# Kernel tuning notes

Hardware: AMD Instinct MI355X
Metric: run time of the kernel (lower is better)

Reference implementation:

```python
import jax, jax.numpy as jnp
import numpy as np

N = 50000        # nodes
E = 800000       # edges
H = 128          # in = hidden = out width
L = 4            # num_layers
BN_EPS = 1e-5


def _bn(x, g, b):
    # training-mode batch norm over the node dimension (biased variance, as torch)
    mu = jnp.mean(x, axis=0)
    var = jnp.mean((x - mu) ** 2, axis=0)
    return (x - mu) * jax.lax.rsqrt(var + BN_EPS) * g + b


def setup_inputs() -> dict:
    key = jax.random.key(0)
    ks = jax.random.split(key, 16)
    s = 0.05
    return {
        "x": jax.random.normal(ks[0], (N, H), dtype=jnp.float32),
        "edge_index": jax.random.randint(ks[1], (2, E), 0, N, dtype=jnp.int32),
        # stacked per-layer MLP params (all layers share dims H->H->H)
        "fc1_w": jax.random.normal(ks[2], (L, H, H), dtype=jnp.float32) * s,
        "fc1_b": jnp.zeros((L, H), dtype=jnp.float32),
        "bn1_g": jnp.ones((L, H), dtype=jnp.float32),
        "bn1_b": jnp.zeros((L, H), dtype=jnp.float32),
        "fc2_w": jax.random.normal(ks[3], (L, H, H), dtype=jnp.float32) * s,
        "fc2_b": jnp.zeros((L, H), dtype=jnp.float32),
        "bn2_g": jnp.ones((L, H), dtype=jnp.float32),
        "bn2_b": jnp.zeros((L, H), dtype=jnp.float32),
        # outer per-layer BatchNorm (intended one-per-GIN-layer)
        "bn3_g": jnp.ones((L, H), dtype=jnp.float32),
        "bn3_b": jnp.zeros((L, H), dtype=jnp.float32),
        # final classifier
        "fc_w": jax.random.normal(ks[4], (H, H), dtype=jnp.float32) * s,
        "fc_b": jnp.zeros((H,), dtype=jnp.float32),
    }


def reference(x, edge_index, fc1_w, fc1_b, bn1_g, bn1_b, fc2_w, fc2_b,
              bn2_g, bn2_b, bn3_g, bn3_b, fc_w, fc_b):
    src = edge_index[0]
    dst = edge_index[1]
    for i in range(L):
        # GINConv, eps=0: h = MLP((1+eps)*x + sum_{j in N(v)} x_j)
        agg = jax.ops.segment_sum(x[src], dst, num_segments=N)  # [N, H]
        h = x + agg
        # MLP: relu(bn1(fc1(h))) -> bn2(fc2(.))
        h = jax.nn.relu(_bn(h @ fc1_w[i].T + fc1_b[i], bn1_g[i], bn1_b[i]))
        h = _bn(h @ fc2_w[i].T + fc2_b[i], bn2_g[i], bn2_b[i])
        # outer BN + ReLU per layer
        x = jax.nn.relu(_bn(h, bn3_g[i], bn3_b[i]))
    return x @ fc_w.T + fc_b  # [N, H]
```

## Files before the change

### kernel.cpp

```cpp
#include <hip/hip_runtime.h>

#define NN 50000
#define HD 128
#define NL 4
#define BN_EPS 1e-5f
#define NTILES 3125
#define MAXDEG 64

typedef __attribute__((ext_vector_type(8))) short short8;
typedef __attribute__((ext_vector_type(4))) float f32x4;
typedef __attribute__((ext_vector_type(4))) uint uint4v;

__device__ inline ushort f2bf(float f){
  uint u = __float_as_uint(f);
  uint r = (u + 0x7fffu + ((u >> 16) & 1u)) >> 16;
  return (ushort)r;
}
__device__ inline float bflo(uint u){ return __uint_as_float(u << 16); }
__device__ inline float bfhi(uint u){ return __uint_as_float(u & 0xffff0000u); }
__device__ inline uint pk2(float lo, float hi){
  return (uint)f2bf(lo) | ((uint)f2bf(hi) << 16);
}

__global__ __launch_bounds__(256) void cast_all(const float* __restrict__ x,
                                                const float* __restrict__ w1,
                                                const float* __restrict__ w2,
                                                const float* __restrict__ wf,
                                                ushort* __restrict__ xb,
                                                ushort* __restrict__ wb){
  const int NX = NN * HD / 4;
  const int NT = NX + 36864;
  int i = blockIdx.x * 256 + threadIdx.x;
  int stride = gridDim.x * 256;
  for (; i < NT; i += stride){
    const float* src; ushort* dst;
    if (i < NX){ src = x + i * 4; dst = xb + i * 4; }
    else {
      int k = i - NX;
      dst = wb + k * 4;
      if (k < 16384)      src = w1 + k * 4;
      else if (k < 32768) src = w2 + (k - 16384) * 4;
      else                src = wf + (k - 32768) * 4;
    }
    float4 v = *(const float4*)src;
    ushort4 r;
    r.x = f2bf(v.x); r.y = f2bf(v.y); r.z = f2bf(v.z); r.w = f2bf(v.w);
    *(ushort4*)dst = r;
  }
}

__global__ void fill1_kernel(const int* __restrict__ dst, int* __restrict__ cnt,
                             int* __restrict__ pos, int E){
  int e = (blockIdx.x * 256 + threadIdx.x) * 4;
  if (e + 4 <= E){
    int4 d = *(const int4*)(dst + e);
    int4 p;
    p.x = atomicAdd(&cnt[d.x], 1);
    p.y = atomicAdd(&cnt[d.y], 1);
    p.z = atomicAdd(&cnt[d.z], 1);
    p.w = atomicAdd(&cnt[d.w], 1);
    *(int4*)(pos + e) = p;
  } else {
    for (; e < E; ++e) pos[e] = atomicAdd(&cnt[dst[e]], 1);
  }
}

__global__ void fill2_kernel(const int* __restrict__ src, const int* __restrict__ dst,
                             const int* __restrict__ pos, int* __restrict__ slots, int E){
  int e = (blockIdx.x * 256 + threadIdx.x) * 4;
  if (e + 4 <= E){
    int4 d = *(const int4*)(dst + e);
    int4 p = *(const int4*)(pos + e);
    int4 s = *(const int4*)(src + e);
    slots[d.x * MAXDEG + p.x] = s.x;
    slots[d.y * MAXDEG + p.y] = s.y;
    slots[d.z * MAXDEG + p.z] = s.z;
    slots[d.w * MAXDEG + p.w] = s.w;
  } else {
    for (; e < E; ++e) slots[dst[e] * MAXDEG + pos[e]] = src[e];
  }
}

__device__ inline void bn_params8(const float* __restrict__ st, const float* __restrict__ gA,
                                  const float* __restrict__ gB, const float* __restrict__ bB,
                                  int mode, float* sS, float* sT){
  int c = threadIdx.x;
  if (c < 128){
    float s0 = 0.f, s1 = 0.f;
#pragma unroll
    for (int k = 0; k < 8; ++k){
      s0 += st[k * 256 + c];
      s1 += st[k * 256 + 128 + c];
    }
    const float invN = 1.f / (float)NN;
    float mu = s0 * invN;
    float var = fmaxf(s1 * invN - mu * mu, 0.f);
    float S, T;
    if (mode == 0){
      S = gA[c] * rsqrtf(var + BN_EPS);
      T = gB[c] - mu * S;
    } else {
      float inv2 = rsqrtf(var + BN_EPS);
      float tt = gA[c] * inv2;
      float inv3 = rsqrtf(tt * tt * var + BN_EPS);
      S = tt * inv3 * gB[c];
      T = bB[c] - mu * S;
    }
    sS[c] = S; sT[c] = T;
  }
}

template<bool AFF>
__global__ __launch_bounds__(512, 6) void aggemm_t(const ushort* __restrict__ xin,
                                                   const int* __restrict__ deg,
                                                   const int* __restrict__ slots,
                                                   const ushort* __restrict__ W,
                                                   const float* __restrict__ bias,
                                                   ushort* __restrict__ Yb,
                                                   float* __restrict__ statsOut,
                                                   const float* __restrict__ statsIn,
                                                   const float* __restrict__ g2,
                                                   const float* __restrict__ g3,
                                                   const float* __restrict__ b3){
  __shared__ uint4v w4[128 * 17];
  __shared__ uint4v a4[2][16 * 17];
  __shared__ float ssum[128];
  __shared__ float ssq[128];
  __shared__ float sS[128];
  __shared__ float sT[128];

  const uint4v* Wg = (const uint4v*)W;
  for (int c = threadIdx.x; c < 2048; c += 512){
    w4[(c >> 4) * 17 + (c & 15)] = Wg[c];
  }
  if (AFF) bn_params8(statsIn, g2, g3, b3, 1, sS, sT);
  if (threadIdx.x < 128){ ssum[threadIdx.x] = 0.f; ssq[threadIdx.x] = 0.f; }
  __syncthreads();

  int wave = threadIdx.x >> 6;
  int lane = threadIdx.x & 63;
  int tl   = wave >> 2;
  int qd   = wave & 3;
  int grp  = lane >> 4;
  int col  = lane & 15;
  int tile = blockIdx.x * 2 + tl;
  bool tv = tile < NTILES;

  float S[8], T[8];
  if (AFF){
#pragma unroll
    for (int k = 0; k < 8; ++k){ S[k] = sS[col * 8 + k]; T[k] = sT[col * 8 + k]; }
  }

  const uint4v* x4 = (const uint4v*)xin;

#define ACC8(v)                                                                 \
  if (AFF){                                                                     \
    a[0]+=fmaxf(bflo((v).x)*S[0]+T[0],0.f); a[1]+=fmaxf(bfhi((v).x)*S[1]+T[1],0.f); \
    a[2]+=fmaxf(bflo((v).y)*S[2]+T[2],0.f); a[3]+=fmaxf(bfhi((v).y)*S[3]+T[3],0.f); \
    a[4]+=fmaxf(bflo((v).z)*S[4]+T[4],0.f); a[5]+=fmaxf(bfhi((v).z)*S[5]+T[5],0.f); \
    a[6]+=fmaxf(bflo((v).w)*S[6]+T[6],0.f); a[7]+=fmaxf(bfhi((v).w)*S[7]+T[7],0.f); \
  } else {                                                                      \
    a[0]+=bflo((v).x); a[1]+=bfhi((v).x); a[2]+=bflo((v).y); a[3]+=bfhi((v).y); \
    a[4]+=bflo((v).z); a[5]+=bfhi((v).z); a[6]+=bflo((v).w); a[7]+=bfhi((v).w); \
  }

  if (tv){
    int node = tile * 16 + qd * 4 + grp;
    int e = deg[node];
    const int* sl = slots + node * MAXDEG;
    float a[8];
    {
      uint4v v = x4[node * 16 + col];
      if (AFF){
        a[0]=fmaxf(bflo(v.x)*S[0]+T[0],0.f); a[1]=fmaxf(bfhi(v.x)*S[1]+T[1],0.f);
        a[2]=fmaxf(bflo(v.y)*S[2]+T[2],0.f); a[3]=fmaxf(bfhi(v.y)*S[3]+T[3],0.f);
        a[4]=fmaxf(bflo(v.z)*S[4]+T[4],0.f); a[5]=fmaxf(bfhi(v.z)*S[5]+T[5],0.f);
        a[6]=fmaxf(bflo(v.w)*S[6]+T[6],0.f); a[7]=fmaxf(bfhi(v.w)*S[7]+T[7],0.f);
      } else {
        a[0]=bflo(v.x); a[1]=bfhi(v.x); a[2]=bflo(v.y); a[3]=bfhi(v.y);
        a[4]=bflo(v.z); a[5]=bfhi(v.z); a[6]=bflo(v.w); a[7]=bfhi(v.w);
      }
    }
    int j = 0;
    for (; j + 8 <= e; j += 8){
      int i0 = sl[j+0], i1 = sl[j+1], i2 = sl[j+2], i3 = sl[j+3];
      int i4 = sl[j+4], i5 = sl[j+5], i6 = sl[j+6], i7 = sl[j+7];
      uint4v v0 = x4[i0 * 16 + col];
      uint4v v1 = x4[i1 * 16 + col];
      uint4v v2 = x4[i2 * 16 + col];
      uint4v v3 = x4[i3 * 16 + col];
      uint4v v4 = x4[i4 * 16 + col];
      uint4v v5 = x4[i5 * 16 + col];
      uint4v v6 = x4[i6 * 16 + col];
      uint4v v7 = x4[i7 * 16 + col];
      ACC8(v0); ACC8(v1); ACC8(v2); ACC8(v3);
      ACC8(v4); ACC8(v5); ACC8(v6); ACC8(v7);
    }
    for (; j + 4 <= e; j += 4){
      int i0 = sl[j+0], i1 = sl[j+1], i2 = sl[j+2], i3 = sl[j+3];
      uint4v v0 = x4[i0 * 16 + col];
      uint4v v1 = x4[i1 * 16 + col];
      uint4v v2 = x4[i2 * 16 + col];
      uint4v v3 = x4[i3 * 16 + col];
      ACC8(v0); ACC8(v1); ACC8(v2); ACC8(v3);
    }
    for (; j < e; ++j){
      uint4v v = x4[sl[j] * 16 + col];
      ACC8(v);
    }
    uint4v o;
    o.x = pk2(a[0], a[1]); o.y = pk2(a[2], a[3]);
    o.z = pk2(a[4], a[5]); o.w = pk2(a[6], a[7]);
    a4[tl][(qd * 4 + grp) * 17 + col] = o;
  }
#undef ACC8
  __syncthreads();

  int m = lane & 15, q = lane >> 4;
  f32x4 acc[2];
  acc[0] = (f32x4)0.f; acc[1] = (f32x4)0.f;

#pragma unroll
  for (int kt = 0; kt < 4; ++kt){
    uint4v t = a4[tl][m * 17 + kt * 4 + q];
    short8 af = *(short8*)&t;
#pragma unroll
    for (int t2 = 0; t2 < 2; ++t2){
      int to = qd * 2 + t2;
      uint4v bw = w4[(to * 16 + m) * 17 + kt * 4 + q];
      acc[t2] = __builtin_amdgcn_mfma_f32_16x16x32_bf16(af, *(short8*)&bw, acc[t2], 0, 0, 0);
    }
  }

#pragma unroll
  for (int t2 = 0; t2 < 2; ++t2){
    int colo = (qd * 2 + t2) * 16 + m;
    float bc = bias[colo];
    float ls = 0.f, lq = 0.f;
    if (tv){
#pragma unroll
      for (int r = 0; r < 4; ++r){
        float v = acc[t2][r] + bc;
        int row = tile * 16 + q * 4 + r;
        __builtin_nontemporal_store(__builtin_bit_cast(ushort, f2bf(v)), Yb + row * 128 + colo);
        ls += v; lq += v * v;
      }
    }
    ls += __shfl_xor(ls, 16); lq += __shfl_xor(lq, 16);
    ls += __shfl_xor(ls, 32); lq += __shfl_xor(lq, 32);
    if (tv && q == 0){ atomicAdd(&ssum[colo], ls); atomicAdd(&ssq[colo], lq); }
  }
  __syncthreads();
  if (threadIdx.x < 128){
    int sb = (blockIdx.x & 7) * 256;
    atomicAdd(&statsOut[sb + threadIdx.x], ssum[threadIdx.x]);
    atomicAdd(&statsOut[sb + 128 + threadIdx.x], ssq[threadIdx.x]);
  }
}

__global__ __launch_bounds__(512, 8) void gemm_kernel(const ushort* __restrict__ A,
                                                   const ushort* __restrict__ W,
                                                   const float* __restrict__ bias,
                                                   ushort* __restrict__ Yb,
                                                   float* __restrict__ Yf,
                                                   float* __restrict__ statsOut,
                                                   const float* __restrict__ statsIn,
                                                   const float* __restrict__ gA,
                                                   const float* __restrict__ gB,
                                                   const float* __restrict__ bB,
                                                   int mode){
  __shared__ uint4v w4[128 * 17];
  __shared__ float ssum[128];
  __shared__ float ssq[128];
  __shared__ float sS[128];
  __shared__ float sT[128];
  const uint4v* Wg = (const uint4v*)W;
  for (int c = threadIdx.x; c < 2048; c += 512){
    w4[(c >> 4) * 17 + (c & 15)] = Wg[c];
  }
  if (statsIn) bn_params8(statsIn, gA, gB, bB, mode, sS, sT);
  if (threadIdx.x < 128){ ssum[threadIdx.x] = 0.f; ssq[threadIdx.x] = 0.f; }
  __syncthreads();

  int wave = threadIdx.x >> 6;
  int lane = threadIdx.x & 63;
  int m = lane & 15, q = lane >> 4;
  int tl   = wave >> 1;
  int half = wave & 1;
  int tile = blockIdx.x * 4 + tl;
  bool tv = tile < NTILES;
  const uint4v* A4 = (const uint4v*)A;

  f32x4 acc[4];
#pragma unroll
  for (int i = 0; i < 4; ++i) acc[i] = (f32x4)0.f;

#pragma unroll
  for (int kt = 0; kt < 4; ++kt){
    short8 af = (short8)0;
    if (tv){
      uint4v t = __builtin_nontemporal_load(A4 + (tile * 16 + m) * 16 + kt * 4 + q);
      if (statsIn){
        int kc = kt * 32 + q * 8;
        uint4v pk;
        pk.x = pk2(fmaxf(bflo(t.x)*sS[kc+0]+sT[kc+0],0.f),
                   fmaxf(bfhi(t.x)*sS[kc+1]+sT[kc+1],0.f));
        pk.y = pk2(fmaxf(bflo(t.y)*sS[kc+2]+sT[kc+2],0.f),
                   fmaxf(bfhi(t.y)*sS[kc+3]+sT[kc+3],0.f));
        pk.z = pk2(fmaxf(bflo(t.z)*sS[kc+4]+sT[kc+4],0.f),
                   fmaxf(bfhi(t.z)*sS[kc+5]+sT[kc+5],0.f));
        pk.w = pk2(fmaxf(bflo(t.w)*sS[kc+6]+sT[kc+6],0.f),
                   fmaxf(bfhi(t.w)*sS[kc+7]+sT[kc+7],0.f));
        t = pk;
      }
      af = *(short8*)&t;
    }
#pragma unroll
    for (int t4 = 0; t4 < 4; ++t4){
      int to = half * 4 + t4;
      uint4v bw = w4[(to * 16 + m) * 17 + kt * 4 + q];
      acc[t4] = __builtin_amdgcn_mfma_f32_16x16x32_bf16(af, *(short8*)&bw, acc[t4], 0, 0, 0);
    }
  }

  bool dost = (statsOut != nullptr);
#pragma unroll
  for (int t4 = 0; t4 < 4; ++t4){
    int col = (half * 4 + t4) * 16 + m;
    float bc = bias[col];
    float ls = 0.f, lq = 0.f;
    if (tv){
#pragma unroll
      for (int r = 0; r < 4; ++r){
        float v = acc[t4][r] + bc;
        int row = tile * 16 + q * 4 + r;
        if (Yb) __builtin_nontemporal_store(__builtin_bit_cast(ushort, f2bf(v)), Yb + row * 128 + col);
        else    __builtin_nontemporal_store(v, Yf + row * 128 + col);
        ls += v; lq += v * v;
      }
    }
    if (dost){
      ls += __shfl_xor(ls, 16); lq += __shfl_xor(lq, 16);
      ls += __shfl_xor(ls, 32); lq += __shfl_xor(lq, 32);
      if (tv && q == 0){ atomicAdd(&ssum[col], ls); atomicAdd(&ssq[col], lq); }
    }
  }
  if (dost){
    __syncthreads();
    if (threadIdx.x < 128){
      int sb = (blockIdx.x & 7) * 256;
      atomicAdd(&statsOut[sb + threadIdx.x], ssum[threadIdx.x]);
      atomicAdd(&statsOut[sb + 128 + threadIdx.x], ssq[threadIdx.x]);
    }
  }
}

extern "C" void kernel_launch(void* const* d_in, const int* in_sizes, int n_in,
                              void* d_out, int out_size, void* d_ws, size_t ws_size,
                              hipStream_t stream) {
  const float* x     = (const float*)d_in[0];
  const int*   ei    = (const int*)d_in[1];
  const float* fc1_w = (const float*)d_in[2];
  const float* fc1_b = (const float*)d_in[3];
  const float* bn1_g = (const float*)d_in[4];
  const float* bn1_b = (const float*)d_in[5];
  const float* fc2_w = (const float*)d_in[6];
  const float* fc2_b = (const float*)d_in[7];
  const float* bn2_g = (const float*)d_in[8];
  const float* bn3_g = (const float*)d_in[10];
  const float* bn3_b = (const float*)d_in[11];
  const float* fc_w  = (const float*)d_in[12];
  const float* fc_b  = (const float*)d_in[13];

  int E = in_sizes[1] / 2;
  const int* srcp = ei;
  const int* dstp = ei + E;

  char* ws = (char*)d_ws;
  int*    cnt    = (int*)(ws + 0);
  float*  stats  = (float*)(ws + 200064);
  int*    pos    = (int*)(ws + 265600);
  int*    slots  = (int*)(ws + 3465600);
  ushort* wb     = (ushort*)(ws + 16265600);
  ushort* xb     = (ushort*)(ws + 16560512);
  ushort* y1b    = (ushort*)(ws + 29360512);
  ushort* y2b    = (ushort*)(ws + 42160512);

  hipMemsetAsync(ws, 0, 265600, stream);

  cast_all<<<2048, 256, 0, stream>>>(x, fc1_w, fc2_w, fc_w, xb, wb);

  const int EB4 = (E / 4 + 255) / 256 + 1;
  fill1_kernel<<<EB4, 256, 0, stream>>>(dstp, cnt, pos, E);
  fill2_kernel<<<EB4, 256, 0, stream>>>(srcp, dstp, pos, slots, E);

  const int ga = (NTILES + 1) / 2;
  const int gb = (NTILES + 3) / 4;

  for (int i = 0; i < NL; ++i){
    if (i == 0){
      aggemm_t<false><<<ga, 512, 0, stream>>>(xb, cnt, slots, wb + i * 16384,
                                              fc1_b + i * 128, y1b,
                                              stats + (i * 2) * 2048,
                                              nullptr, nullptr, nullptr, nullptr);
    } else {
      aggemm_t<true><<<ga, 512, 0, stream>>>(y2b, cnt, slots, wb + i * 16384,
                                             fc1_b + i * 128, y1b,
                                             stats + (i * 2) * 2048,
                                             stats + ((i - 1) * 2 + 1) * 2048,
                                             bn2_g + (i - 1) * 128,
                                             bn3_g + (i - 1) * 128,
                                             bn3_b + (i - 1) * 128);
    }
    gemm_kernel<<<gb, 512, 0, stream>>>(y1b, wb + 65536 + i * 16384, fc2_b + i * 128,
                                        y2b, nullptr, stats + (i * 2 + 1) * 2048,
                                        stats + (i * 2) * 2048, bn1_g + i * 128,
                                        bn1_b + i * 128, nullptr, 0);
  }

  gemm_kernel<<<gb, 512, 0, stream>>>(y2b, wb + 131072, fc_b,
                                      nullptr, (float*)d_out, nullptr,
                                      stats + 7 * 2048, bn2_g + 384,
                                      bn3_g + 384, bn3_b + 384, 1);
}
```

Before: 467.7 us.

## Split aggregation from GEMM and store features in column-sliced layout

The fused aggregate+GEMM kernel becomes a standalone gather kernel. It works on four 32-column slices of a sliced feature layout, so each slice's gathered rows are compact and likely to stay cache-resident. The fc1 GEMM now runs as a separate gemm_kernel launch that reads the sliced layout. The fc2 GEMM writes its output sliced for the next layer's gather. Stats binning grows from 8 to 64 bins to reduce atomic contention. The cost is an extra kernel launch per layer and an extra round trip of the aggregated features through memory.

After: 512.2 us. 1.1x slower.

```diff
diff --git a/kernel.cpp b/kernel.cpp
--- a/kernel.cpp
+++ b/kernel.cpp
@@ -6,6 +6,7 @@
 #define BN_EPS 1e-5f
 #define NTILES 3125
 #define MAXDEG 64
+#define SBIN 64
 
 typedef __attribute__((ext_vector_type(8))) short short8;
 typedef __attribute__((ext_vector_type(4))) float f32x4;
@@ -26,7 +27,7 @@
                                                 const float* __restrict__ w1,
                                                 const float* __restrict__ w2,
                                                 const float* __restrict__ wf,
-                                                ushort* __restrict__ xb,
+                                                ushort* __restrict__ xs,
                                                 ushort* __restrict__ wb){
   const int NX = NN * HD / 4;
   const int NT = NX + 36864;
@@ -34,8 +35,12 @@
   int stride = gridDim.x * 256;
   for (; i < NT; i += stride){
     const float* src; ushort* dst;
-    if (i < NX){ src = x + i * 4; dst = xb + i * 4; }
-    else {
+    if (i < NX){
+      int node = i >> 5;
+      int c0 = (i & 31) * 4;
+      src = x + i * 4;
+      dst = xs + ((c0 >> 5) * NN + node) * 32 + (c0 & 31);
+    } else {
       int k = i - NX;
       dst = wb + k * 4;
       if (k < 16384)      src = w1 + k * 4;
@@ -81,14 +86,14 @@
   }
 }
 
-__device__ inline void bn_params8(const float* __restrict__ st, const float* __restrict__ gA,
-                                  const float* __restrict__ gB, const float* __restrict__ bB,
-                                  int mode, float* sS, float* sT){
+__device__ inline void bn_params(const float* __restrict__ st, const float* __restrict__ gA,
+                                 const float* __restrict__ gB, const float* __restrict__ bB,
+                                 int mode, float* sS, float* sT){
   int c = threadIdx.x;
   if (c < 128){
     float s0 = 0.f, s1 = 0.f;
-#pragma unroll
-    for (int k = 0; k < 8; ++k){
+#pragma unroll 8
+    for (int k = 0; k < SBIN; ++k){
       s0 += st[k * 256 + c];
       s1 += st[k * 256 + 128 + c];
     }
@@ -111,152 +116,90 @@
 }
 
 template<bool AFF>
-__global__ __launch_bounds__(512, 6) void aggemm_t(const ushort* __restrict__ xin,
-                                                   const int* __restrict__ deg,
-                                                   const int* __restrict__ slots,
-                                                   const ushort* __restrict__ W,
-                                                   const float* __restrict__ bias,
-                                                   ushort* __restrict__ Yb,
-                                                   float* __restrict__ statsOut,
-                                                   const float* __restrict__ statsIn,
-                                                   const float* __restrict__ g2,
-                                                   const float* __restrict__ g3,
-                                                   const float* __restrict__ b3){
-  __shared__ uint4v w4[128 * 17];
-  __shared__ uint4v a4[2][16 * 17];
-  __shared__ float ssum[128];
-  __shared__ float ssq[128];
+__global__ __launch_bounds__(256) void aggs_t(const ushort* __restrict__ xs,
+                                              const int* __restrict__ deg,
+                                              const int* __restrict__ slots,
+                                              const float* __restrict__ statsIn,
+                                              const float* __restrict__ g2,
+                                              const float* __restrict__ g3,
+                                              const float* __restrict__ b3,
+                                              ushort* __restrict__ hs){
   __shared__ float sS[128];
   __shared__ float sT[128];
-
-  const uint4v* Wg = (const uint4v*)W;
-  for (int c = threadIdx.x; c < 2048; c += 512){
-    w4[(c >> 4) * 17 + (c & 15)] = Wg[c];
-  }
-  if (AFF) bn_params8(statsIn, g2, g3, b3, 1, sS, sT);
-  if (threadIdx.x < 128){ ssum[threadIdx.x] = 0.f; ssq[threadIdx.x] = 0.f; }
-  __syncthreads();
-
-  int wave = threadIdx.x >> 6;
-  int lane = threadIdx.x & 63;
-  int tl   = wave >> 2;
-  int qd   = wave & 3;
-  int grp  = lane >> 4;
-  int col  = lane & 15;
-  int tile = blockIdx.x * 2 + tl;
-  bool tv = tile < NTILES;
+  if (AFF){
+    bn_params(statsIn, g2, g3, b3, 1, sS, sT);
+    __syncthreads();
+  }
+  int slice = blockIdx.x & 3;
+  int nb    = blockIdx.x >> 2;
+  int gid   = threadIdx.x >> 2;
+  int li    = threadIdx.x & 3;
+  int node  = nb * 64 + gid;
+  if (node >= NN) return;
 
   float S[8], T[8];
   if (AFF){
-#pragma unroll
-    for (int k = 0; k < 8; ++k){ S[k] = sS[col * 8 + k]; T[k] = sT[col * 8 + k]; }
-  }
-
-  const uint4v* x4 = (const uint4v*)xin;
-
-#define ACC8(v)                                                                 \
-  if (AFF){                                                                     \
+    int cb = slice * 32 + li * 8;
+#pragma unroll
+    for (int k = 0; k < 8; ++k){ S[k] = sS[cb + k]; T[k] = sT[cb + k]; }
+  }
+
+  const uint4v* x4 = (const uint4v*)xs;
+  const int base = slice * (NN * 4);
+  int e = deg[node];
+  const int* sl = slots + node * MAXDEG;
+
+  float a[8];
+#define UNPK(v)                                                                  \
+  if (AFF){                                                                      \
     a[0]+=fmaxf(bflo((v).x)*S[0]+T[0],0.f); a[1]+=fmaxf(bfhi((v).x)*S[1]+T[1],0.f); \
     a[2]+=fmaxf(bflo((v).y)*S[2]+T[2],0.f); a[3]+=fmaxf(bfhi((v).y)*S[3]+T[3],0.f); \
     a[4]+=fmaxf(bflo((v).z)*S[4]+T[4],0.f); a[5]+=fmaxf(bfhi((v).z)*S[5]+T[5],0.f); \
     a[6]+=fmaxf(bflo((v).w)*S[6]+T[6],0.f); a[7]+=fmaxf(bfhi((v).w)*S[7]+T[7],0.f); \
-  } else {                                                                      \
-    a[0]+=bflo((v).x); a[1]+=bfhi((v).x); a[2]+=bflo((v).y); a[3]+=bfhi((v).y); \
-    a[4]+=bflo((v).z); a[5]+=bfhi((v).z); a[6]+=bflo((v).w); a[7]+=bfhi((v).w); \
-  }
-
-  if (tv){
-    int node = tile * 16 + qd * 4 + grp;
-    int e = deg[node];
-    const int* sl = slots + node * MAXDEG;
-    float a[8];
-    {
-      uint4v v = x4[node * 16 + col];
-      if (AFF){
-        a[0]=fmaxf(bflo(v.x)*S[0]+T[0],0.f); a[1]=fmaxf(bfhi(v.x)*S[1]+T[1],0.f);
-        a[2]=fmaxf(bflo(v.y)*S[2]+T[2],0.f); a[3]=fmaxf(bfhi(v.y)*S[3]+T[3],0.f);
-        a[4]=fmaxf(bflo(v.z)*S[4]+T[4],0.f); a[5]=fmaxf(bfhi(v.z)*S[5]+T[5],0.f);
-        a[6]=fmaxf(bflo(v.w)*S[6]+T[6],0.f); a[7]=fmaxf(bfhi(v.w)*S[7]+T[7],0.f);
-      } else {
-        a[0]=bflo(v.x); a[1]=bfhi(v.x); a[2]=bflo(v.y); a[3]=bfhi(v.y);
-        a[4]=bflo(v.z); a[5]=bfhi(v.z); a[6]=bflo(v.w); a[7]=bfhi(v.w);
-      }
-    }
-    int j = 0;
-    for (; j + 8 <= e; j += 8){
-      int i0 = sl[j+0], i1 = sl[j+1], i2 = sl[j+2], i3 = sl[j+3];
-      int i4 = sl[j+4], i5 = sl[j+5], i6 = sl[j+6], i7 = sl[j+7];
-      uint4v v0 = x4[i0 * 16 + col];
-      uint4v v1 = x4[i1 * 16 + col];
-      uint4v v2 = x4[i2 * 16 + col];
-      uint4v v3 = x4[i3 * 16 + col];
-      uint4v v4 = x4[i4 * 16 + col];
-      uint4v v5 = x4[i5 * 16 + col];
-      uint4v v6 = x4[i6 * 16 + col];
-      uint4v v7 = x4[i7 * 16 + col];
-      ACC8(v0); ACC8(v1); ACC8(v2); ACC8(v3);
-      ACC8(v4); ACC8(v5); ACC8(v6); ACC8(v7);
-    }
-    for (; j + 4 <= e; j += 4){
-      int i0 = sl[j+0], i1 = sl[j+1], i2 = sl[j+2], i3 = sl[j+3];
-      uint4v v0 = x4[i0 * 16 + col];
-      uint4v v1 = x4[i1 * 16 + col];
-      uint4v v2 = x4[i2 * 16 + col];
-      uint4v v3 = x4[i3 * 16 + col];
-      ACC8(v0); ACC8(v1); ACC8(v2); ACC8(v3);
-    }
-    for (; j < e; ++j){
-      uint4v v = x4[sl[j] * 16 + col];
-      ACC8(v);
-    }
-    uint4v o;
-    o.x = pk2(a[0], a[1]); o.y = pk2(a[2], a[3]);
-    o.z = pk2(a[4], a[5]); o.w = pk2(a[6], a[7]);
-    a4[tl][(qd * 4 + grp) * 17 + col] = o;
-  }
-#undef ACC8
-  __syncthreads();
-
-  int m = lane & 15, q = lane >> 4;
-  f32x4 acc[2];
-  acc[0] = (f32x4)0.f; acc[1] = (f32x4)0.f;
-
-#pragma unroll
-  for (int kt = 0; kt < 4; ++kt){
-    uint4v t = a4[tl][m * 17 + kt * 4 + q];
-    short8 af = *(short8*)&t;
-#pragma unroll
-    for (int t2 = 0; t2 < 2; ++t2){
-      int to = qd * 2 + t2;
-      uint4v bw = w4[(to * 16 + m) * 17 + kt * 4 + q];
-      acc[t2] = __builtin_amdgcn_mfma_f32_16x16x32_bf16(af, *(short8*)&bw, acc[t2], 0, 0, 0);
-    }
-  }
-
-#pragma unroll
-  for (int t2 = 0; t2 < 2; ++t2){
-    int colo = (qd * 2 + t2) * 16 + m;
-    float bc = bias[colo];
-    float ls = 0.f, lq = 0.f;
-    if (tv){
-#pragma unroll
-      for (int r = 0; r < 4; ++r){
-        float v = acc[t2][r] + bc;
-        int row = tile * 16 + q * 4 + r;
-        __builtin_nontemporal_store(__builtin_bit_cast(ushort, f2bf(v)), Yb + row * 128 + colo);
-        ls += v; lq += v * v;
-      }
-    }
-    ls += __shfl_xor(ls, 16); lq += __shfl_xor(lq, 16);
-    ls += __shfl_xor(ls, 32); lq += __shfl_xor(lq, 32);
-    if (tv && q == 0){ atomicAdd(&ssum[colo], ls); atomicAdd(&ssq[colo], lq); }
-  }
-  __syncthreads();
-  if (threadIdx.x < 128){
-    int sb = (blockIdx.x & 7) * 256;
-    atomicAdd(&statsOut[sb + threadIdx.x], ssum[threadIdx.x]);
-    atomicAdd(&statsOut[sb + 128 + threadIdx.x], ssq[threadIdx.x]);
-  }
+  } else {                                                                       \
+    a[0]+=bflo((v).x); a[1]+=bfhi((v).x); a[2]+=bflo((v).y); a[3]+=bfhi((v).y);  \
+    a[4]+=bflo((v).z); a[5]+=bfhi((v).z); a[6]+=bflo((v).w); a[7]+=bfhi((v).w);  \
+  }
+
+#pragma unroll
+  for (int k = 0; k < 8; ++k) a[k] = 0.f;
+  {
+    uint4v v = x4[base + node * 4 + li];
+    UNPK(v);
+  }
+  int j = 0;
+  for (; j + 8 <= e; j += 8){
+    int i0 = sl[j+0], i1 = sl[j+1], i2 = sl[j+2], i3 = sl[j+3];
+    int i4 = sl[j+4], i5 = sl[j+5], i6 = sl[j+6], i7 = sl[j+7];
+    uint4v v0 = x4[base + i0 * 4 + li];
+    uint4v v1 = x4[base + i1 * 4 + li];
+    uint4v v2 = x4[base + i2 * 4 + li];
+    uint4v v3 = x4[base + i3 * 4 + li];
+    uint4v v4 = x4[base + i4 * 4 + li];
+    uint4v v5 = x4[base + i5 * 4 + li];
+    uint4v v6 = x4[base + i6 * 4 + li];
+    uint4v v7 = x4[base + i7 * 4 + li];
+    UNPK(v0); UNPK(v1); UNPK(v2); UNPK(v3);
+    UNPK(v4); UNPK(v5); UNPK(v6); UNPK(v7);
+  }
+  for (; j + 4 <= e; j += 4){
+    int i0 = sl[j+0], i1 = sl[j+1], i2 = sl[j+2], i3 = sl[j+3];
+    uint4v v0 = x4[base + i0 * 4 + li];
+    uint4v v1 = x4[base + i1 * 4 + li];
+    uint4v v2 = x4[base + i2 * 4 + li];
+    uint4v v3 = x4[base + i3 * 4 + li];
+    UNPK(v0); UNPK(v1); UNPK(v2); UNPK(v3);
+  }
+  for (; j < e; ++j){
+    uint4v v = x4[base + sl[j] * 4 + li];
+    UNPK(v);
+  }
+#undef UNPK
+
+  uint4v o;
+  o.x = pk2(a[0], a[1]); o.y = pk2(a[2], a[3]);
+  o.z = pk2(a[4], a[5]); o.w = pk2(a[6], a[7]);
+  __builtin_nontemporal_store(o, (uint4v*)hs + base + node * 4 + li);
 }
 
 __global__ __launch_bounds__(512, 8) void gemm_kernel(const ushort* __restrict__ A,
@@ -269,7 +212,7 @@
                                                    const float* __restrict__ gA,
                                                    const float* __restrict__ gB,
                                                    const float* __restrict__ bB,
-                                                   int mode){
+                                                   int mode, int isl, int osl){
   __shared__ uint4v w4[128 * 17];
   __shared__ float ssum[128];
   __shared__ float ssq[128];
@@ -279,7 +222,7 @@
   for (int c = threadIdx.x; c < 2048; c += 512){
     w4[(c >> 4) * 17 + (c & 15)] = Wg[c];
   }
-  if (statsIn) bn_params8(statsIn, gA, gB, bB, mode, sS, sT);
+  if (statsIn) bn_params(statsIn, gA, gB, bB, mode, sS, sT);
   if (threadIdx.x < 128){ ssum[threadIdx.x] = 0.f; ssq[threadIdx.x] = 0.f; }
   __syncthreads();
 
@@ -296,13 +239,17 @@
 #pragma unroll
   for (int i = 0; i < 4; ++i) acc[i] = (f32x4)0.f;
 
+  int row = tile * 16 + m;
 #pragma unroll
   for (int kt = 0; kt < 4; ++kt){
     short8 af = (short8)0;
     if (tv){
-      uint4v t = __builtin_nontemporal_load(A4 + (tile * 16 + m) * 16 + kt * 4 + q);
+      int c = kt * 4 + q;
+      const uint4v* ap = isl ? (A4 + ((c >> 2) * (NN * 4) + row * 4 + (c & 3)))
+                             : (A4 + row * 16 + c);
+      uint4v t = __builtin_nontemporal_load(ap);
       if (statsIn){
-        int kc = kt * 32 + q * 8;
+        int kc = c * 8;
         uint4v pk;
         pk.x = pk2(fmaxf(bflo(t.x)*sS[kc+0]+sT[kc+0],0.f),
                    fmaxf(bfhi(t.x)*sS[kc+1]+sT[kc+1],0.f));
@@ -334,9 +281,14 @@
 #pragma unroll
       for (int r = 0; r < 4; ++r){
         float v = acc[t4][r] + bc;
-        int row = tile * 16 + q * 4 + r;
-        if (Yb) __builtin_nontemporal_store(__builtin_bit_cast(ushort, f2bf(v)), Yb + row * 128 + col);
-        else    __builtin_nontemporal_store(v, Yf + row * 128 + col);
+        int rw = tile * 16 + q * 4 + r;
+        if (Yb){
+          int addr = osl ? (((col >> 5) * NN + rw) * 32 + (col & 31))
+                         : (rw * 128 + col);
+          __builtin_nontemporal_store(__builtin_bit_cast(ushort, f2bf(v)), Yb + addr);
+        } else {
+          __builtin_nontemporal_store(v, Yf + rw * 128 + col);
+        }
         ls += v; lq += v * v;
       }
     }
@@ -349,7 +301,7 @@
   if (dost){
     __syncthreads();
     if (threadIdx.x < 128){
-      int sb = (blockIdx.x & 7) * 256;
+      int sb = (blockIdx.x & (SBIN - 1)) * 256;
       atomicAdd(&statsOut[sb + threadIdx.x], ssum[threadIdx.x]);
       atomicAdd(&statsOut[sb + 128 + threadIdx.x], ssq[threadIdx.x]);
     }
@@ -380,47 +332,47 @@
   char* ws = (char*)d_ws;
   int*    cnt    = (int*)(ws + 0);
   float*  stats  = (float*)(ws + 200064);
-  int*    pos    = (int*)(ws + 265600);
-  int*    slots  = (int*)(ws + 3465600);
-  ushort* wb     = (ushort*)(ws + 16265600);
-  ushort* xb     = (ushort*)(ws + 16560512);
-  ushort* y1b    = (ushort*)(ws + 29360512);
-  ushort* y2b    = (ushort*)(ws + 42160512);
-
-  hipMemsetAsync(ws, 0, 265600, stream);
-
-  cast_all<<<2048, 256, 0, stream>>>(x, fc1_w, fc2_w, fc_w, xb, wb);
+  int*    pos    = (int*)(ws + 724352);
+  int*    slots  = (int*)(ws + 3924352);
+  ushort* wb     = (ushort*)(ws + 16724352);
+  ushort* xs     = (ushort*)(ws + 17019264);
+  ushort* hs     = (ushort*)(ws + 29819264);
+  ushort* y1b    = (ushort*)(ws + 42619264);
+  ushort* y2s    = (ushort*)(ws + 55419264);
+
+  hipMemsetAsync(ws, 0, 724352, stream);
+
+  cast_all<<<2048, 256, 0, stream>>>(x, fc1_w, fc2_w, fc_w, xs, wb);
 
   const int EB4 = (E / 4 + 255) / 256 + 1;
   fill1_kernel<<<EB4, 256, 0, stream>>>(dstp, cnt, pos, E);
   fill2_kernel<<<EB4, 256, 0, stream>>>(srcp, dstp, pos, slots, E);
 
-  const int ga = (NTILES + 1) / 2;
+  const int gaggs = ((NN + 63) / 64) * 4;
   const int gb = (NTILES + 3) / 4;
 
   for (int i = 0; i < NL; ++i){
     if (i == 0){
-      aggemm_t<false><<<ga, 512, 0, stream>>>(xb, cnt, slots, wb + i * 16384,
-                                              fc1_b + i * 128, y1b,
-                                              stats + (i * 2) * 2048,
-                                              nullptr, nullptr, nullptr, nullptr);
+      aggs_t<false><<<gaggs, 256, 0, stream>>>(xs, cnt, slots,
+                                               nullptr, nullptr, nullptr, nullptr, hs);
     } else {
-      aggemm_t<true><<<ga, 512, 0, stream>>>(y2b, cnt, slots, wb + i * 16384,
-                                             fc1_b + i * 128, y1b,
-                                             stats + (i * 2) * 2048,
-                                             stats + ((i - 1) * 2 + 1) * 2048,
-                                             bn2_g + (i - 1) * 128,
-                                             bn3_g + (i - 1) * 128,
-                                             bn3_b + (i - 1) * 128);
-    }
+      aggs_t<true><<<gaggs, 256, 0, stream>>>(y2s, cnt, slots,
+                                              stats + ((i - 1) * 2 + 1) * 16384,
+                                              bn2_g + (i - 1) * 128,
+                                              bn3_g + (i - 1) * 128,
+                                              bn3_b + (i - 1) * 128, hs);
+    }
+    gemm_kernel<<<gb, 512, 0, stream>>>(hs, wb + i * 16384, fc1_b + i * 128,
+                                        y1b, nullptr, stats + (i * 2) * 16384,
+                                        nullptr, nullptr, nullptr, nullptr, 0, 1, 0);
     gemm_kernel<<<gb, 512, 0, stream>>>(y1b, wb + 65536 + i * 16384, fc2_b + i * 128,
-                                        y2b, nullptr, stats + (i * 2 + 1) * 2048,
-                                        stats + (i * 2) * 2048, bn1_g + i * 128,
-                                        bn1_b + i * 128, nullptr, 0);
-  }
-
-  gemm_kernel<<<gb, 512, 0, stream>>>(y2b, wb + 131072, fc_b,
+                                        y2s, nullptr, stats + (i * 2 + 1) * 16384,
+                                        stats + (i * 2) * 16384, bn1_g + i * 128,
+                                        bn1_b + i * 128, nullptr, 0, 0, 1);
+  }
+
+  gemm_kernel<<<gb, 512, 0, stream>>>(y2s, wb + 131072, fc_b,
                                       nullptr, (float*)d_out, nullptr,
-                                      stats + 7 * 2048, bn2_g + 384,
-                                      bn3_g + 384, bn3_b + 384, 1);
-}
+                                      stats + 7 * 16384, bn2_g + 384,
+                                      bn3_g + 384, bn3_b + 384, 1, 1, 0);
+}
```
